# Kernel tuning notes

Measured on AMD Instinct MI355X. Metric: run time of the kernel, lower is better.

Reference implementation:

```python
import jax, jax.numpy as jnp
import numpy as np

MARGIN = 1.0  # from init_kwargs
B, H, W, P = 64, 512, 640, 100000


def setup_inputs() -> dict:
    key = jax.random.key(0)
    k0, k1, k2, k3, k4, k5 = jax.random.split(key, 6)
    return {
        "inp": jax.random.normal(k0, (B, 1, H, W), dtype=jnp.float32),
        "x_A": jax.random.randint(k1, (B, P), 0, W, dtype=jnp.int32),
        "y_A": jax.random.randint(k2, (B, P), 0, H, dtype=jnp.int32),
        "x_B": jax.random.randint(k3, (B, P), 0, W, dtype=jnp.int32),
        "y_B": jax.random.randint(k4, (B, P), 0, H, dtype=jnp.int32),
        "ordinal": jax.random.randint(k5, (B, P), 0, 3, dtype=jnp.int32),
    }


def reference(inp, x_A, y_A, x_B, y_B, ordinal):
    # inp: [B,1,H,W]; point coords: [B,P]; ordinal in {0,1,2} -> gt in {-1,0,1}
    depth = inp[:, 0]                                   # [B,H,W]
    bidx = jnp.arange(depth.shape[0])[:, None]          # [B,1]
    z_A = depth[bidx, y_A, x_A]                         # [B,P] gather
    z_B = depth[bidx, y_B, x_B]                         # [B,P] gather
    gt = (ordinal - 1).astype(depth.dtype)              # {-1,0,1}
    mask = jnp.abs(gt)
    zd = z_A - z_B
    m = jnp.asarray(MARGIN, depth.dtype)
    # ordered pairs: log(1+exp(-min(gt*zd, m))); equal pairs: max(zd^2, m^2)
    loss = mask * jnp.log(1.0 + jnp.exp(-jnp.minimum(gt * zd, m))) \
         + (1.0 - mask) * jnp.maximum(zd * zd, m * m)
    n_point_total = depth.shape[0] * x_A.shape[1]
    return jnp.sum(loss) / n_point_total
```

## Files before the change

kernel.cpp:

```cpp
#include <hip/hip_runtime.h>


constexpr int B = 64;
constexpr int H = 512;
constexpr int W = 640;
constexpr int P = 100000;
constexpr int N4 = (B * P) / 4;
constexpr float INV_N = 1.0f / (float)(B * P);
constexpr float MARGIN = 1.0f;

__device__ __forceinline__ float loss_elem(const float* __restrict__ d,
                                           int ya, int xa, int yb, int xb, int od) {
    float za = d[ya * W + xa];
    float zb = d[yb * W + xb];
    float zd = za - zb;
    float gt = (float)(od - 1);
    float mask = fabsf(gt);
    float t = fminf(gt * zd, MARGIN);
    float l_rank = __logf(1.0f + __expf(-t));
    float l_eq = fmaxf(zd * zd, MARGIN * MARGIN);
    return mask * l_rank + (1.0f - mask) * l_eq;
}

__global__ __launch_bounds__(256) void rdc_kernel(
        const float* __restrict__ depth,
        const int4* __restrict__ xA, const int4* __restrict__ yA,
        const int4* __restrict__ xB, const int4* __restrict__ yB,
        const int4* __restrict__ ord,
        float* __restrict__ out) {
    int i = blockIdx.x * blockDim.x + threadIdx.x;
    float acc = 0.0f;
    if (i < N4) {
        int b = i / (P / 4);
        const float* d = depth + (size_t)b * (H * W);
        int4 xa = xA[i], ya = yA[i], xb = xB[i], yb = yB[i], od = ord[i];
        acc += loss_elem(d, ya.x, xa.x, yb.x, xb.x, od.x);
        acc += loss_elem(d, ya.y, xa.y, yb.y, xb.y, od.y);
        acc += loss_elem(d, ya.z, xa.z, yb.z, xb.z, od.z);
        acc += loss_elem(d, ya.w, xa.w, yb.w, xb.w, od.w);
    }

    #pragma unroll
    for (int off = 32; off > 0; off >>= 1)
        acc += __shfl_down(acc, off, 64);

    __shared__ float wsum[4];
    int lane = threadIdx.x & 63;
    int wid  = threadIdx.x >> 6;
    if (lane == 0) wsum[wid] = acc;
    __syncthreads();
    if (wid == 0) {
        float v = (lane < 4) ? wsum[lane] : 0.0f;
        #pragma unroll
        for (int off = 2; off > 0; off >>= 1)
            v += __shfl_down(v, off, 64);
        if (lane == 0)
            atomicAdd(out, v * INV_N);
    }
}

extern "C" void kernel_launch(void* const* d_in, const int* in_sizes, int n_in,
                              void* d_out, int out_size, void* d_ws, size_t ws_size,
                              hipStream_t stream) {
    const float* depth = (const float*)d_in[0];
    const int4* xA = (const int4*)d_in[1];
    const int4* yA = (const int4*)d_in[2];
    const int4* xB = (const int4*)d_in[3];
    const int4* yB = (const int4*)d_in[4];
    const int4* ord = (const int4*)d_in[5];
    float* out = (float*)d_out;

    hipMemsetAsync(out, 0, sizeof(float), stream);

    int blocks = (N4 + 255) / 256;
    rdc_kernel<<<blocks, 256, 0, stream>>>(depth, xA, yA, xB, yB, ord, out);
}
```

Measured before the change: 277.0 us.

## Stage depth slabs in LDS as bf16 stripes and gather from shared memory

Each block now owns one batch image and a quarter of its points. It keeps point offsets in registers while streaming the image in 48-row stripes into LDS, packed as bf16, then gathers z values from LDS instead of issuing random global loads. It also swaps the atomic accumulation for per-block partials reduced by a second kernel, and uses nontemporal index loads. The bf16 rounding changes numerical precision, and each block re-reads a full image slab, with four blocks reading each image, in exchange for coalesced traffic.

```diff
diff --git a/kernel.cpp b/kernel.cpp
--- a/kernel.cpp
+++ b/kernel.cpp
@@ -5,73 +5,150 @@
 constexpr int H = 512;
 constexpr int W = 640;
 constexpr int P = 100000;
-constexpr int N4 = (B * P) / 4;
+constexpr int SEGS = 4;
+constexpr int SEGP = P / SEGS;
+constexpr int NT = 512;
+constexpr int K = (SEGP + NT - 1) / NT;
+constexpr int TAIL_T = SEGP - (K - 1) * NT;
+constexpr int SROWS = 48;
+constexpr int NS = (H + SROWS - 1) / SROWS;
+constexpr int SELEMS = SROWS * W;
+constexpr int NBLK = B * SEGS;
 constexpr float INV_N = 1.0f / (float)(B * P);
-constexpr float MARGIN = 1.0f;
 
-__device__ __forceinline__ float loss_elem(const float* __restrict__ d,
-                                           int ya, int xa, int yb, int xb, int od) {
-    float za = d[ya * W + xa];
-    float zb = d[yb * W + xb];
-    float zd = za - zb;
-    float gt = (float)(od - 1);
-    float mask = fabsf(gt);
-    float t = fminf(gt * zd, MARGIN);
-    float l_rank = __logf(1.0f + __expf(-t));
-    float l_eq = fmaxf(zd * zd, MARGIN * MARGIN);
-    return mask * l_rank + (1.0f - mask) * l_eq;
-}
+typedef float vfloat4 __attribute__((ext_vector_type(4)));
 
-__global__ __launch_bounds__(256) void rdc_kernel(
+__global__ __launch_bounds__(NT, 2) void rdc_kernel(
         const float* __restrict__ depth,
-        const int4* __restrict__ xA, const int4* __restrict__ yA,
-        const int4* __restrict__ xB, const int4* __restrict__ yB,
-        const int4* __restrict__ ord,
-        float* __restrict__ out) {
-    int i = blockIdx.x * blockDim.x + threadIdx.x;
+        const int* __restrict__ xA, const int* __restrict__ yA,
+        const int* __restrict__ xB, const int* __restrict__ yB,
+        const int* __restrict__ ord,
+        float* __restrict__ partials) {
+    __shared__ unsigned short stripe[SELEMS];
+    __shared__ float wsum[8];
+
+    int j = blockIdx.x;
+    int x = j & 7;
+    int g = j >> 3;
+    int b = (g >> 2) * 8 + x;
+    int c = g & 3;
+    int t = threadIdx.x;
+
+    const float* slab = depth + (size_t)b * (H * W);
+    int base_pt = b * P + c * SEGP;
+
+    int offA[K], offB[K];
+    float zA[K], zB[K];
+    unsigned rankW[2] = {0u, 0u};
+    unsigned signW[2] = {0u, 0u};
+    #pragma unroll
+    for (int k = 0; k < K; ++k) {
+        int pl = k * NT + t;
+        if (k == K - 1 && pl >= SEGP) pl = SEGP - 1;
+        int gi = base_pt + pl;
+        int xa = __builtin_nontemporal_load(&xA[gi]);
+        int ya = __builtin_nontemporal_load(&yA[gi]);
+        int xb = __builtin_nontemporal_load(&xB[gi]);
+        int yb = __builtin_nontemporal_load(&yB[gi]);
+        int od = __builtin_nontemporal_load(&ord[gi]);
+        offA[k] = ya * W + xa;
+        offB[k] = yb * W + xb;
+        rankW[k >> 5] |= (unsigned)(od != 1) << (k & 31);
+        signW[k >> 5] |= (unsigned)(od == 2) << (k & 31);
+        zA[k] = 0.0f;
+        zB[k] = 0.0f;
+    }
+
+    for (int s = 0; s < NS; ++s) {
+        int base = s * SELEMS;
+        int rows = (s == NS - 1) ? (H - s * SROWS) : SROWS;
+        unsigned span = (unsigned)(rows * W);
+        int nv4 = (int)(span >> 2);
+
+        __syncthreads();
+        for (int i4 = t; i4 < nv4; i4 += NT) {
+            vfloat4 v = *(const vfloat4*)(slab + base + (i4 << 2));
+            unsigned u0 = (__builtin_bit_cast(unsigned, v.x) + 0x8000u) >> 16;
+            unsigned u1 = (__builtin_bit_cast(unsigned, v.y) + 0x8000u) >> 16;
+            unsigned u2 = (__builtin_bit_cast(unsigned, v.z) + 0x8000u) >> 16;
+            unsigned u3 = (__builtin_bit_cast(unsigned, v.w) + 0x8000u) >> 16;
+            uint2 pk;
+            pk.x = u0 | (u1 << 16);
+            pk.y = u2 | (u3 << 16);
+            *(uint2*)&stripe[i4 << 2] = pk;
+        }
+        __syncthreads();
+
+        #pragma unroll
+        for (int k = 0; k < K; ++k) {
+            unsigned la = (unsigned)(offA[k] - base);
+            if (la < span)
+                zA[k] = __builtin_bit_cast(float, (unsigned)stripe[la] << 16);
+            unsigned lb = (unsigned)(offB[k] - base);
+            if (lb < span)
+                zB[k] = __builtin_bit_cast(float, (unsigned)stripe[lb] << 16);
+        }
+    }
+
+    float tailf = (t < TAIL_T) ? 1.0f : 0.0f;
     float acc = 0.0f;
-    if (i < N4) {
-        int b = i / (P / 4);
-        const float* d = depth + (size_t)b * (H * W);
-        int4 xa = xA[i], ya = yA[i], xb = xB[i], yb = yB[i], od = ord[i];
-        acc += loss_elem(d, ya.x, xa.x, yb.x, xb.x, od.x);
-        acc += loss_elem(d, ya.y, xa.y, yb.y, xb.y, od.y);
-        acc += loss_elem(d, ya.z, xa.z, yb.z, xb.z, od.z);
-        acc += loss_elem(d, ya.w, xa.w, yb.w, xb.w, od.w);
+    #pragma unroll
+    for (int k = 0; k < K; ++k) {
+        float zd = zA[k] - zB[k];
+        unsigned rb = (rankW[k >> 5] >> (k & 31)) & 1u;
+        unsigned sb = (signW[k >> 5] >> (k & 31)) & 1u;
+        float gt = sb ? 1.0f : -1.0f;
+        float lr = __logf(1.0f + __expf(-fminf(gt * zd, 1.0f)));
+        float le = fmaxf(zd * zd, 1.0f);
+        float l = rb ? lr : le;
+        if (k == K - 1) l *= tailf;
+        acc += l;
     }
 
     #pragma unroll
-    for (int off = 32; off > 0; off >>= 1)
-        acc += __shfl_down(acc, off, 64);
+    for (int o = 32; o > 0; o >>= 1)
+        acc += __shfl_down(acc, o, 64);
+    int lane = t & 63;
+    int wid  = t >> 6;
+    if (lane == 0) wsum[wid] = acc;
+    __syncthreads();
+    if (wid == 0 && lane == 0) {
+        float v = 0.0f;
+        #pragma unroll
+        for (int w = 0; w < 8; ++w) v += wsum[w];
+        partials[j] = v;
+    }
+}
 
+__global__ __launch_bounds__(256) void rdc_finalize(
+        const float* __restrict__ partials, float* __restrict__ out, int n) {
+    float acc = 0.0f;
+    for (int k = threadIdx.x; k < n; k += 256)
+        acc += partials[k];
+    #pragma unroll
+    for (int o = 32; o > 0; o >>= 1)
+        acc += __shfl_down(acc, o, 64);
     __shared__ float wsum[4];
     int lane = threadIdx.x & 63;
     int wid  = threadIdx.x >> 6;
     if (lane == 0) wsum[wid] = acc;
     __syncthreads();
-    if (wid == 0) {
-        float v = (lane < 4) ? wsum[lane] : 0.0f;
-        #pragma unroll
-        for (int off = 2; off > 0; off >>= 1)
-            v += __shfl_down(v, off, 64);
-        if (lane == 0)
-            atomicAdd(out, v * INV_N);
-    }
+    if (wid == 0 && lane == 0)
+        out[0] = (wsum[0] + wsum[1] + wsum[2] + wsum[3]) * INV_N;
 }
 
 extern "C" void kernel_launch(void* const* d_in, const int* in_sizes, int n_in,
                               void* d_out, int out_size, void* d_ws, size_t ws_size,
                               hipStream_t stream) {
     const float* depth = (const float*)d_in[0];
-    const int4* xA = (const int4*)d_in[1];
-    const int4* yA = (const int4*)d_in[2];
-    const int4* xB = (const int4*)d_in[3];
-    const int4* yB = (const int4*)d_in[4];
-    const int4* ord = (const int4*)d_in[5];
+    const int* xA = (const int*)d_in[1];
+    const int* yA = (const int*)d_in[2];
+    const int* xB = (const int*)d_in[3];
+    const int* yB = (const int*)d_in[4];
+    const int* ord = (const int*)d_in[5];
     float* out = (float*)d_out;
 
-    hipMemsetAsync(out, 0, sizeof(float), stream);
-
-    int blocks = (N4 + 255) / 256;
-    rdc_kernel<<<blocks, 256, 0, stream>>>(depth, xA, yA, xB, yB, ord, out);
+    float* partials = (float*)d_ws;
+    rdc_kernel<<<NBLK, NT, 0, stream>>>(depth, xA, yA, xB, yB, ord, partials);
+    rdc_finalize<<<1, 256, 0, stream>>>(partials, out, NBLK);
 }
```

Measured after the change: 321.4 us. 16.1% more time.
